# Kernel tuning notes

Measured on AMD Instinct MI355X. Metric: run time of the kernel, lower is better.

Reference implementation:

```python
import jax, jax.numpy as jnp
import numpy as np

DIM = 768
NUM_HEADS = 12
HEAD_DIM = DIM // NUM_HEADS
ALL_HEAD_DIM = HEAD_DIM * NUM_HEADS
SCALE = HEAD_DIM ** -0.5


def setup_inputs() -> dict:
    key = jax.random.key(0)
    k1, k2, k3, k4 = jax.random.split(key, 4)
    B, N = 8, 1024
    x = jax.random.normal(k1, (B, N, DIM), dtype=jnp.float32)
    # qkv_bias=False -> no qkv bias; proj has bias (nn.Linear default)
    w_qkv = jax.random.normal(k2, (DIM, 3 * ALL_HEAD_DIM), dtype=jnp.float32) * (DIM ** -0.5)
    w_proj = jax.random.normal(k3, (ALL_HEAD_DIM, DIM), dtype=jnp.float32) * (ALL_HEAD_DIM ** -0.5)
    b_proj = jax.random.normal(k4, (DIM,), dtype=jnp.float32) * 0.02
    return {"x": x, "w_qkv": w_qkv, "w_proj": w_proj, "b_proj": b_proj}


def reference(x, w_qkv, w_proj, b_proj):
    B, N, C = x.shape
    qkv = (x @ w_qkv).reshape(B, N, 3, NUM_HEADS, HEAD_DIM)
    qkv = jnp.transpose(qkv, (2, 0, 3, 1, 4))  # [3, B, H, N, D]
    q, k, v = qkv[0], qkv[1], qkv[2]
    attn = jax.nn.softmax(jnp.einsum('bhnd,bhmd->bhnm', q * SCALE, k), axis=-1)
    out = jnp.einsum('bhnm,bhmd->bhnd', attn, v)  # [B, H, N, D]
    out = jnp.transpose(out, (0, 2, 1, 3)).reshape(B, N, ALL_HEAD_DIM)
    return out @ w_proj + b_proj
```

## Files before the change

kernel.cpp:

```cpp
#include <hip/hip_runtime.h>
#include <hip/hip_bf16.h>

#define NH 12
#define HD 64
#define SEQ 1024
#define BATCH 8
#define DIM 768
#define QKVN 2304
#define ROWS 8192

typedef __bf16 bf16x8 __attribute__((ext_vector_type(8)));
typedef float f32x4 __attribute__((ext_vector_type(4)));
typedef unsigned short u16x8 __attribute__((ext_vector_type(8)));
typedef unsigned short u16x4 __attribute__((ext_vector_type(4)));
typedef short s16x4 __attribute__((ext_vector_type(4)));

__device__ __forceinline__ unsigned short f2bf(float f) {
  union { float f; unsigned int u; } c; c.f = f;
  unsigned int u = c.u;
  u += 0x7fffu + ((u >> 16) & 1u);
  return (unsigned short)(u >> 16);
}

__device__ __forceinline__ unsigned int pk_bf16(float a, float b) {
  union { __hip_bfloat162 h; unsigned int w; } u;
  u.h = __float22bfloat162_rn(float2{a, b});
  return u.w;
}

__device__ __forceinline__ float exp2_fast(float x) {
  float r;
  asm("v_exp_f32 %0, %1" : "=v"(r) : "v"(x));
  return r;
}

__device__ __forceinline__ void gload_lds16(const unsigned short* g, unsigned short* l) {
  __builtin_amdgcn_global_load_lds(
      (const __attribute__((address_space(1))) void*)g,
      (__attribute__((address_space(3))) void*)l, 16, 0, 0);
}

__device__ __forceinline__ void tr_tile(const float* __restrict__ src, unsigned short* __restrict__ dst,
                                        int R, int C, int bx, int by, float tile[32][33]) {
  int tx = threadIdx.x & 31, ty = threadIdx.x >> 5;
  int c0 = bx * 32, r0 = by * 32;
#pragma unroll
  for (int i = 0; i < 4; ++i)
    tile[ty + i * 8][tx] = src[(size_t)(r0 + ty + i * 8) * C + c0 + tx];
  __syncthreads();
#pragma unroll
  for (int i = 0; i < 4; ++i)
    dst[(size_t)(c0 + ty + i * 8) * R + r0 + tx] = f2bf(tile[tx][ty + i * 8]);
}

__global__ void prep_kernel(const float* __restrict__ x, unsigned short* __restrict__ xb,
                            const float* __restrict__ w_qkv, unsigned short* __restrict__ wqkvT,
                            const float* __restrict__ w_proj, unsigned short* __restrict__ wprojT) {
  __shared__ float tile[32][33];
  int blk = blockIdx.x;
  if (blk < 6144) {
    int i = blk * 256 + threadIdx.x;
    float4 v = ((const float4*)x)[i];
    unsigned int lo = pk_bf16(v.x, v.y), hi = pk_bf16(v.z, v.w);
    union { unsigned int w[2]; u16x4 o; } u; u.w[0] = lo; u.w[1] = hi;
    ((u16x4*)xb)[i] = u.o;
  } else if (blk < 6144 + 1728) {
    int t = blk - 6144;
    tr_tile(w_qkv, wqkvT, DIM, QKVN, t % 72, t / 72, tile);
  } else {
    int t = blk - 6144 - 1728;
    tr_tile(w_proj, wprojT, DIM, DIM, t % 24, t / 24, tile);
  }
}

template <bool BF16_OUT, bool SCALE_Q>
__global__ __launch_bounds__(256, 3) void gemm192(
    const unsigned short* __restrict__ A, const unsigned short* __restrict__ BT,
    void* __restrict__ Cout, const float* __restrict__ bias,
    int M, int N, int K, int nbyXCD) {
  __shared__ unsigned short As[2][128 * 32];
  __shared__ unsigned short Bs[2][192 * 32];
  const int tid = threadIdx.x;
  const int wave = tid >> 6, lane = tid & 63, quad = lane >> 4, l16 = lane & 15;
  const int wm = wave >> 1, wn = wave & 1;
  const int g = blockIdx.x & 7, bi = blockIdx.x >> 3;
  const int by = g * nbyXCD + (bi % nbyXCD);
  const int bx = bi / nbyXCD;
  const int bm = by * 128, bn = bx * 192;

  const int r0 = tid >> 2, kc0 = (tid & 3) * 8;
  const unsigned short* Ag = A + (size_t)(bm + r0) * K + kc0;
  const unsigned short* Bg = BT + (size_t)(bn + r0) * K + kc0;
  unsigned short* AsB = &As[0][0];
  unsigned short* BsB = &Bs[0][0];
  const int wdst = (tid & ~63) * 8;

#define STAGE_G(kt, b) do {                                                   \
    int koff_ = (kt) * 32;                                                    \
    gload_lds16(Ag + koff_,                    AsB + (b) * 4096 + wdst);      \
    gload_lds16(Ag + koff_ + (size_t)64 * K,   AsB + (b) * 4096 + wdst + 2048);\
    gload_lds16(Bg + koff_,                    BsB + (b) * 6144 + wdst);      \
    gload_lds16(Bg + koff_ + (size_t)64 * K,   BsB + (b) * 6144 + wdst + 2048);\
    gload_lds16(Bg + koff_ + (size_t)128 * K,  BsB + (b) * 6144 + wdst + 4096);\
  } while (0)

  f32x4 zero4 = {0.f, 0.f, 0.f, 0.f};
  f32x4 acc[4][6];
#pragma unroll
  for (int i = 0; i < 4; ++i)
#pragma unroll
    for (int j = 0; j < 6; ++j) acc[i][j] = zero4;

  const int nkt = K >> 5;
  STAGE_G(0, 0);
  for (int kt = 0; kt < nkt; ++kt) {
    __syncthreads();
    if (kt + 1 < nkt) STAGE_G(kt + 1, (kt + 1) & 1);
    const unsigned short* Ab = AsB + (kt & 1) * 4096;
    const unsigned short* Bb = BsB + (kt & 1) * 6144;
    bf16x8 af[4], bf[6];
#pragma unroll
    for (int mt = 0; mt < 4; ++mt)
      af[mt] = *(const bf16x8*)&Ab[(wm * 64 + mt * 16 + l16) * 32 + quad * 8];
#pragma unroll
    for (int nt = 0; nt < 6; ++nt)
      bf[nt] = *(const bf16x8*)&Bb[(wn * 96 + nt * 16 + l16) * 32 + quad * 8];
#pragma unroll
    for (int mt = 0; mt < 4; ++mt)
#pragma unroll
      for (int nt = 0; nt < 6; ++nt)
        acc[mt][nt] = __builtin_amdgcn_mfma_f32_16x16x32_bf16(af[mt], bf[nt], acc[mt][nt], 0, 0, 0);
  }
#undef STAGE_G

#pragma unroll
  for (int mt = 0; mt < 4; ++mt)
#pragma unroll
    for (int nt = 0; nt < 6; ++nt) {
      int col = bn + wn * 96 + nt * 16 + l16;
      float bv = BF16_OUT ? 0.f : bias[col];
      float scl = (SCALE_Q && col < DIM) ? 0.18033688011112042f : 1.0f;
#pragma unroll
      for (int r = 0; r < 4; ++r) {
        int row = bm + wm * 64 + mt * 16 + quad * 4 + r;
        float v = acc[mt][nt][r];
        if (BF16_OUT)
          ((unsigned short*)Cout)[(size_t)row * N + col] = f2bf(v * scl);
        else
          ((float*)Cout)[(size_t)row * N + col] = v + bv;
      }
    }
}

__global__ __launch_bounds__(256, 5) void gemm64_proj(
    const unsigned short* __restrict__ A, const unsigned short* __restrict__ BT,
    float* __restrict__ Cout, const float* __restrict__ bias,
    int M, int N, int K, int nbyXCD) {
  __shared__ unsigned short As[2][128 * 32];
  __shared__ unsigned short Bs[2][64 * 32];
  const int tid = threadIdx.x;
  const int wave = tid >> 6, lane = tid & 63, quad = lane >> 4, l16 = lane & 15;
  const int g = blockIdx.x & 7, bi = blockIdx.x >> 3;
  const int by = g * nbyXCD + (bi % nbyXCD);
  const int bx = bi / nbyXCD;
  const int bm = by * 128, bn = bx * 64;

  const int r0 = tid >> 2, kc0 = (tid & 3) * 8;
  const unsigned short* Ag = A + (size_t)(bm + r0) * K + kc0;
  const unsigned short* Bg = BT + (size_t)(bn + r0) * K + kc0;
  unsigned short* AsB = &As[0][0];
  unsigned short* BsB = &Bs[0][0];
  const int wdst = (tid & ~63) * 8;

#define STAGE_P(kt, b) do {                                                    \
    int koff_ = (kt) * 32;                                                     \
    gload_lds16(Ag + koff_,                  AsB + (b) * 4096 + wdst);         \
    gload_lds16(Ag + koff_ + (size_t)64 * K, AsB + (b) * 4096 + wdst + 2048);  \
    gload_lds16(Bg + koff_,                  BsB + (b) * 2048 + wdst);         \
  } while (0)

  f32x4 zero4 = {0.f, 0.f, 0.f, 0.f};
  f32x4 acc[2][4];
#pragma unroll
  for (int i = 0; i < 2; ++i)
#pragma unroll
    for (int j = 0; j < 4; ++j) acc[i][j] = zero4;

  const int nkt = K >> 5;
  STAGE_P(0, 0);
  for (int kt = 0; kt < nkt; ++kt) {
    __syncthreads();
    if (kt + 1 < nkt) STAGE_P(kt + 1, (kt + 1) & 1);
    const unsigned short* Ab = AsB + (kt & 1) * 4096;
    const unsigned short* Bb = BsB + (kt & 1) * 2048;
    bf16x8 af[2], bf[4];
#pragma unroll
    for (int mt = 0; mt < 2; ++mt)
      af[mt] = *(const bf16x8*)&Ab[(wave * 32 + mt * 16 + l16) * 32 + quad * 8];
#pragma unroll
    for (int nt = 0; nt < 4; ++nt)
      bf[nt] = *(const bf16x8*)&Bb[(nt * 16 + l16) * 32 + quad * 8];
#pragma unroll
    for (int mt = 0; mt < 2; ++mt)
#pragma unroll
      for (int nt = 0; nt < 4; ++nt)
        acc[mt][nt] = __builtin_amdgcn_mfma_f32_16x16x32_bf16(af[mt], bf[nt], acc[mt][nt], 0, 0, 0);
  }
#undef STAGE_P

#pragma unroll
  for (int mt = 0; mt < 2; ++mt)
#pragma unroll
    for (int nt = 0; nt < 4; ++nt) {
      int col = bn + nt * 16 + l16;
      float bv = bias[col];
#pragma unroll
      for (int r = 0; r < 4; ++r) {
        int row = bm + wave * 32 + mt * 16 + quad * 4 + r;
        Cout[(size_t)row * N + col] = acc[mt][nt][r] + bv;
      }
    }
}

#define VS 76
__global__ __launch_bounds__(512, 6) void attn_kernel(
    const unsigned short* __restrict__ qkv, unsigned short* __restrict__ out) {
  __shared__ unsigned short Ks[2][64 * 64];
  __shared__ unsigned short Vts[2][64 * VS];

  const int tid = threadIdx.x;
  const int wave = tid >> 6, lane = tid & 63, quad = lane >> 4, l16 = lane & 15;
  const int x = blockIdx.x;
  const int qt = (x >> 3) & 7;
  const int bh = (x & 7) + 8 * (x >> 6);
  const int b = bh / NH, h = bh % NH;
  const int qcol = h * HD, kcol = DIM + h * HD, vcol = 2 * DIM + h * HD;
  const int rowQ0 = b * SEQ + qt * 128;
  const int rowKV0 = b * SEQ;

  const int kk_s = tid >> 8, rem_s = tid & 255, n_s = rem_s >> 2, kc_s = rem_s & 3;
  const unsigned short* kgp = qkv + (size_t)(rowKV0 + n_s) * QKVN + kcol + kk_s * 32 + kc_s * 8;
  unsigned short* klp = &Ks[0][0] + (tid & ~63) * 8;
  const int vn = tid & 63, vd0 = (tid >> 6) * 8;
  const unsigned short* vgp = qkv + (size_t)(rowKV0 + vn) * QKVN + vcol + vd0;

  bf16x8 qf[2];
  {
    const unsigned short* qp = qkv + (size_t)(rowQ0 + wave * 16 + l16) * QKVN + qcol + quad * 8;
    qf[0] = *(const bf16x8*)qp;
    qf[1] = *(const bf16x8*)(qp + 32);
  }

  gload_lds16(kgp, klp);
  {
    u16x8 v0 = *(const u16x8*)vgp;
    unsigned short* vb = &Vts[0][0];
#pragma unroll
    for (int e = 0; e < 8; ++e)
      vb[(vd0 + e) * VS + vn] = v0[e];
  }

  f32x4 zero4 = {0.f, 0.f, 0.f, 0.f};
  f32x4 o[4];
#pragma unroll
  for (int dt = 0; dt < 4; ++dt) o[dt] = zero4;
  float lsum = 0.f;

  for (int jt = 0; jt < 16; ++jt) {
    __syncthreads();
    u16x8 vnext;
    if (jt < 15) {
      gload_lds16(kgp + (size_t)(jt + 1) * 64 * QKVN, klp + ((jt + 1) & 1) * 4096);
      vnext = *(const u16x8*)(vgp + (size_t)(jt + 1) * 64 * QKVN);
    }

    const unsigned short* Kb = &Ks[jt & 1][0];
    const unsigned short* Vb = &Vts[jt & 1][0];

    f32x4 s[4];
#pragma unroll
    for (int nt = 0; nt < 4; ++nt) s[nt] = zero4;
    __builtin_amdgcn_s_setprio(1);
#pragma unroll
    for (int kk = 0; kk < 2; ++kk)
#pragma unroll
      for (int nt = 0; nt < 4; ++nt) {
        bf16x8 kf = *(const bf16x8*)&Kb[kk * 2048 + (nt * 16 + l16) * 32 + quad * 8];
        s[nt] = __builtin_amdgcn_mfma_f32_16x16x32_bf16(kf, qf[kk], s[nt], 0, 0, 0);
      }
    __builtin_amdgcn_s_setprio(0);

    s16x4 pf[4];
#pragma unroll
    for (int nt = 0; nt < 4; ++nt) {
      float p0 = exp2_fast(s[nt][0]);
      float p1 = exp2_fast(s[nt][1]);
      float p2 = exp2_fast(s[nt][2]);
      float p3 = exp2_fast(s[nt][3]);
      lsum += (p0 + p1) + (p2 + p3);
      union { unsigned int w[2]; s16x4 v; } u;
      u.w[0] = pk_bf16(p0, p1);
      u.w[1] = pk_bf16(p2, p3);
      pf[nt] = u.v;
    }

    __builtin_amdgcn_s_setprio(1);
#pragma unroll
    for (int nt = 0; nt < 4; ++nt)
#pragma unroll
      for (int dt = 0; dt < 4; ++dt) {
        s16x4 vv = *(const s16x4*)&Vb[(dt * 16 + l16) * VS + nt * 16 + quad * 4];
        o[dt] = __builtin_amdgcn_mfma_f32_16x16x16bf16_1k(pf[nt], vv, o[dt], 0, 0, 0);
      }
    __builtin_amdgcn_s_setprio(0);

    if (jt < 15) {
      unsigned short* vb = &Vts[(jt + 1) & 1][0];
#pragma unroll
      for (int e = 0; e < 8; ++e)
        vb[(vd0 + e) * VS + vn] = vnext[e];
    }
  }

  float l = lsum;
  l += __shfl_xor(l, 16);
  l += __shfl_xor(l, 32);
#pragma unroll
  for (int r = 0; r < 4; ++r) {
    float inv = 1.f / __shfl(l, quad * 4 + r);
    int row = rowQ0 + wave * 16 + quad * 4 + r;
#pragma unroll
    for (int dt = 0; dt < 4; ++dt)
      out[(size_t)row * DIM + h * HD + dt * 16 + l16] = f2bf(o[dt][r] * inv);
  }
}

extern "C" void kernel_launch(void* const* d_in, const int* in_sizes, int n_in,
                              void* d_out, int out_size, void* d_ws, size_t ws_size,
                              hipStream_t stream) {
  const float* x = (const float*)d_in[0];
  const float* w_qkv = (const float*)d_in[1];
  const float* w_proj = (const float*)d_in[2];
  const float* b_proj = (const float*)d_in[3];
  float* outp = (float*)d_out;

  unsigned short* xb = (unsigned short*)d_ws;
  unsigned short* wqkvT = xb + (size_t)ROWS * DIM;
  unsigned short* wprojT = wqkvT + (size_t)QKVN * DIM;
  unsigned short* qkvb = wprojT + (size_t)DIM * DIM;
  unsigned short* attnb = xb;

  prep_kernel<<<dim3(6144 + 1728 + 576), 256, 0, stream>>>(x, xb, w_qkv, wqkvT, w_proj, wprojT);
  gemm192<true, true><<<dim3(768), 256, 0, stream>>>(xb, wqkvT, qkvb, nullptr, ROWS, QKVN, DIM, 8);
  attn_kernel<<<dim3(8 * 96), 512, 0, stream>>>(qkvb, attnb);
  gemm64_proj<<<dim3(768), 256, 0, stream>>>(attnb, wprojT, outp, b_proj, ROWS, DIM, DIM, 8);
}
```

Measured before the change: 178.5 us.

## Double K-tile depth in proj GEMM with swizzled LDS and widen attention KV tile

The projection GEMM now stages 64-wide K slices instead of 32, using an XOR-swizzled LDS layout to avoid bank conflicts. This halves the number of barriers and iterations per tile. The attention kernel now processes 128 keys per iteration instead of 64, halving the loop trip count and its syncs. In exchange both kernels use more LDS and registers, and their occupancy bounds are lowered to match.

Result: slower. 182.1 us (+2.0%).

```diff
diff --git a/kernel.cpp b/kernel.cpp
--- a/kernel.cpp
+++ b/kernel.cpp
@@ -152,12 +152,12 @@
     }
 }
 
-__global__ __launch_bounds__(256, 5) void gemm64_proj(
+__global__ __launch_bounds__(256, 4) void gemm64_proj(
     const unsigned short* __restrict__ A, const unsigned short* __restrict__ BT,
     float* __restrict__ Cout, const float* __restrict__ bias,
     int M, int N, int K, int nbyXCD) {
-  __shared__ unsigned short As[2][128 * 32];
-  __shared__ unsigned short Bs[2][64 * 32];
+  __shared__ unsigned short As[2][128 * 64];
+  __shared__ unsigned short Bs[2][64 * 64];
   const int tid = threadIdx.x;
   const int wave = tid >> 6, lane = tid & 63, quad = lane >> 4, l16 = lane & 15;
   const int g = blockIdx.x & 7, bi = blockIdx.x >> 3;
@@ -165,18 +165,22 @@
   const int bx = bi / nbyXCD;
   const int bm = by * 128, bn = bx * 64;
 
-  const int r0 = tid >> 2, kc0 = (tid & 3) * 8;
-  const unsigned short* Ag = A + (size_t)(bm + r0) * K + kc0;
-  const unsigned short* Bg = BT + (size_t)(bn + r0) * K + kc0;
+  const int r0 = tid >> 3;
+  const int csw = ((tid & 7) ^ (r0 & 7)) * 8;
+  const unsigned short* Ag = A + (size_t)(bm + r0) * K + csw;
+  const unsigned short* Bg = BT + (size_t)(bn + r0) * K + csw;
   unsigned short* AsB = &As[0][0];
   unsigned short* BsB = &Bs[0][0];
   const int wdst = (tid & ~63) * 8;
 
-#define STAGE_P(kt, b) do {                                                    \
-    int koff_ = (kt) * 32;                                                     \
-    gload_lds16(Ag + koff_,                  AsB + (b) * 4096 + wdst);         \
-    gload_lds16(Ag + koff_ + (size_t)64 * K, AsB + (b) * 4096 + wdst + 2048);  \
-    gload_lds16(Bg + koff_,                  BsB + (b) * 2048 + wdst);         \
+#define STAGE_P(kt, b) do {                                                     \
+    int koff_ = (kt) * 64;                                                      \
+    gload_lds16(Ag + koff_,                   AsB + (b) * 8192 + wdst);         \
+    gload_lds16(Ag + koff_ + (size_t)32 * K,  AsB + (b) * 8192 + wdst + 2048);  \
+    gload_lds16(Ag + koff_ + (size_t)64 * K,  AsB + (b) * 8192 + wdst + 4096);  \
+    gload_lds16(Ag + koff_ + (size_t)96 * K,  AsB + (b) * 8192 + wdst + 6144);  \
+    gload_lds16(Bg + koff_,                   BsB + (b) * 4096 + wdst);         \
+    gload_lds16(Bg + koff_ + (size_t)32 * K,  BsB + (b) * 4096 + wdst + 2048);  \
   } while (0)
 
   f32x4 zero4 = {0.f, 0.f, 0.f, 0.f};
@@ -186,25 +190,29 @@
 #pragma unroll
     for (int j = 0; j < 4; ++j) acc[i][j] = zero4;
 
-  const int nkt = K >> 5;
+  const int nkt = K >> 6;
   STAGE_P(0, 0);
   for (int kt = 0; kt < nkt; ++kt) {
     __syncthreads();
     if (kt + 1 < nkt) STAGE_P(kt + 1, (kt + 1) & 1);
-    const unsigned short* Ab = AsB + (kt & 1) * 4096;
-    const unsigned short* Bb = BsB + (kt & 1) * 2048;
-    bf16x8 af[2], bf[4];
-#pragma unroll
-    for (int mt = 0; mt < 2; ++mt)
-      af[mt] = *(const bf16x8*)&Ab[(wave * 32 + mt * 16 + l16) * 32 + quad * 8];
-#pragma unroll
-    for (int nt = 0; nt < 4; ++nt)
-      bf[nt] = *(const bf16x8*)&Bb[(nt * 16 + l16) * 32 + quad * 8];
-#pragma unroll
-    for (int mt = 0; mt < 2; ++mt)
+    const unsigned short* Ab = AsB + (kt & 1) * 8192;
+    const unsigned short* Bb = BsB + (kt & 1) * 4096;
+#pragma unroll
+    for (int kk = 0; kk < 2; ++kk) {
+      const int pc = ((kk * 4 + quad) ^ (l16 & 7)) * 8;
+      bf16x8 af[2], bf[4];
+#pragma unroll
+      for (int mt = 0; mt < 2; ++mt)
+        af[mt] = *(const bf16x8*)&Ab[(wave * 32 + mt * 16 + l16) * 64 + pc];
 #pragma unroll
       for (int nt = 0; nt < 4; ++nt)
-        acc[mt][nt] = __builtin_amdgcn_mfma_f32_16x16x32_bf16(af[mt], bf[nt], acc[mt][nt], 0, 0, 0);
+        bf[nt] = *(const bf16x8*)&Bb[(nt * 16 + l16) * 64 + pc];
+#pragma unroll
+      for (int mt = 0; mt < 2; ++mt)
+#pragma unroll
+        for (int nt = 0; nt < 4; ++nt)
+          acc[mt][nt] = __builtin_amdgcn_mfma_f32_16x16x32_bf16(af[mt], bf[nt], acc[mt][nt], 0, 0, 0);
+    }
   }
 #undef STAGE_P
 
@@ -222,11 +230,11 @@
     }
 }
 
-#define VS 76
-__global__ __launch_bounds__(512, 6) void attn_kernel(
+#define VS2 132
+__global__ __launch_bounds__(512, 4) void attn_kernel(
     const unsigned short* __restrict__ qkv, unsigned short* __restrict__ out) {
-  __shared__ unsigned short Ks[2][64 * 64];
-  __shared__ unsigned short Vts[2][64 * VS];
+  __shared__ unsigned short Ks[2][2 * 128 * 32];
+  __shared__ unsigned short Vts[2][64 * VS2];
 
   const int tid = threadIdx.x;
   const int wave = tid >> 6, lane = tid & 63, quad = lane >> 4, l16 = lane & 15;
@@ -238,10 +246,10 @@
   const int rowQ0 = b * SEQ + qt * 128;
   const int rowKV0 = b * SEQ;
 
-  const int kk_s = tid >> 8, rem_s = tid & 255, n_s = rem_s >> 2, kc_s = rem_s & 3;
-  const unsigned short* kgp = qkv + (size_t)(rowKV0 + n_s) * QKVN + kcol + kk_s * 32 + kc_s * 8;
+  const int n_s = tid >> 2, kc_s = tid & 3;
+  const unsigned short* kgp = qkv + (size_t)(rowKV0 + n_s) * QKVN + kcol + kc_s * 8;
   unsigned short* klp = &Ks[0][0] + (tid & ~63) * 8;
-  const int vn = tid & 63, vd0 = (tid >> 6) * 8;
+  const int vn = tid & 127, vd0 = (tid >> 7) * 16;
   const unsigned short* vgp = qkv + (size_t)(rowKV0 + vn) * QKVN + vcol + vd0;
 
   bf16x8 qf[2];
@@ -252,12 +260,16 @@
   }
 
   gload_lds16(kgp, klp);
+  gload_lds16(kgp + 32, klp + 4096);
   {
-    u16x8 v0 = *(const u16x8*)vgp;
+    u16x8 v0a = *(const u16x8*)vgp;
+    u16x8 v0b = *(const u16x8*)(vgp + 8);
     unsigned short* vb = &Vts[0][0];
 #pragma unroll
-    for (int e = 0; e < 8; ++e)
-      vb[(vd0 + e) * VS + vn] = v0[e];
+    for (int e = 0; e < 8; ++e) {
+      vb[(vd0 + e) * VS2 + vn] = v0a[e];
+      vb[(vd0 + 8 + e) * VS2 + vn] = v0b[e];
+    }
   }
 
   f32x4 zero4 = {0.f, 0.f, 0.f, 0.f};
@@ -266,33 +278,37 @@
   for (int dt = 0; dt < 4; ++dt) o[dt] = zero4;
   float lsum = 0.f;
 
-  for (int jt = 0; jt < 16; ++jt) {
+  for (int jt = 0; jt < 8; ++jt) {
     __syncthreads();
-    u16x8 vnext;
-    if (jt < 15) {
-      gload_lds16(kgp + (size_t)(jt + 1) * 64 * QKVN, klp + ((jt + 1) & 1) * 4096);
-      vnext = *(const u16x8*)(vgp + (size_t)(jt + 1) * 64 * QKVN);
+    u16x8 vna, vnb;
+    if (jt < 7) {
+      const size_t goff = (size_t)(jt + 1) * 128 * QKVN;
+      unsigned short* kd = klp + ((jt + 1) & 1) * 8192;
+      gload_lds16(kgp + goff, kd);
+      gload_lds16(kgp + goff + 32, kd + 4096);
+      vna = *(const u16x8*)(vgp + goff);
+      vnb = *(const u16x8*)(vgp + goff + 8);
     }
 
     const unsigned short* Kb = &Ks[jt & 1][0];
     const unsigned short* Vb = &Vts[jt & 1][0];
 
-    f32x4 s[4];
-#pragma unroll
-    for (int nt = 0; nt < 4; ++nt) s[nt] = zero4;
+    f32x4 s[8];
+#pragma unroll
+    for (int nt = 0; nt < 8; ++nt) s[nt] = zero4;
     __builtin_amdgcn_s_setprio(1);
 #pragma unroll
     for (int kk = 0; kk < 2; ++kk)
 #pragma unroll
-      for (int nt = 0; nt < 4; ++nt) {
-        bf16x8 kf = *(const bf16x8*)&Kb[kk * 2048 + (nt * 16 + l16) * 32 + quad * 8];
+      for (int nt = 0; nt < 8; ++nt) {
+        bf16x8 kf = *(const bf16x8*)&Kb[kk * 4096 + (nt * 16 + l16) * 32 + quad * 8];
         s[nt] = __builtin_amdgcn_mfma_f32_16x16x32_bf16(kf, qf[kk], s[nt], 0, 0, 0);
       }
     __builtin_amdgcn_s_setprio(0);
 
-    s16x4 pf[4];
-#pragma unroll
-    for (int nt = 0; nt < 4; ++nt) {
+    s16x4 pf[8];
+#pragma unroll
+    for (int nt = 0; nt < 8; ++nt) {
       float p0 = exp2_fast(s[nt][0]);
       float p1 = exp2_fast(s[nt][1]);
       float p2 = exp2_fast(s[nt][2]);
@@ -306,19 +322,21 @@
 
     __builtin_amdgcn_s_setprio(1);
 #pragma unroll
-    for (int nt = 0; nt < 4; ++nt)
+    for (int nt = 0; nt < 8; ++nt)
 #pragma unroll
       for (int dt = 0; dt < 4; ++dt) {
-        s16x4 vv = *(const s16x4*)&Vb[(dt * 16 + l16) * VS + nt * 16 + quad * 4];
+        s16x4 vv = *(const s16x4*)&Vb[(dt * 16 + l16) * VS2 + nt * 16 + quad * 4];
         o[dt] = __builtin_amdgcn_mfma_f32_16x16x16bf16_1k(pf[nt], vv, o[dt], 0, 0, 0);
       }
     __builtin_amdgcn_s_setprio(0);
 
-    if (jt < 15) {
+    if (jt < 7) {
       unsigned short* vb = &Vts[(jt + 1) & 1][0];
 #pragma unroll
-      for (int e = 0; e < 8; ++e)
-        vb[(vd0 + e) * VS + vn] = vnext[e];
+      for (int e = 0; e < 8; ++e) {
+        vb[(vd0 + e) * VS2 + vn] = vna[e];
+        vb[(vd0 + 8 + e) * VS2 + vn] = vnb[e];
+      }
     }
   }
 
```

## Triple-buffer LDS staging in QKV and proj GEMMs with explicit vmcnt waits

Applied to the files above, without the earlier changes.

Both bf16 GEMM kernels go from double-buffered to triple-buffered LDS, with tiles prefetched two k-steps ahead. The full __syncthreads (which waits for all outstanding loads) is replaced by a partial s_waitcnt vmcnt plus s_barrier, so the next tile's global-to-LDS loads stay in flight across the barrier. This is meant to hide global memory latency better. In exchange it uses 1.5x the LDS, so the proj kernel's launch bound drops from 5 to 3 blocks per CU and occupancy may fall.

Result: slower. 187.7 us (+5.2%).

```diff
diff --git a/kernel.cpp b/kernel.cpp
--- a/kernel.cpp
+++ b/kernel.cpp
@@ -78,8 +78,8 @@
     const unsigned short* __restrict__ A, const unsigned short* __restrict__ BT,
     void* __restrict__ Cout, const float* __restrict__ bias,
     int M, int N, int K, int nbyXCD) {
-  __shared__ unsigned short As[2][128 * 32];
-  __shared__ unsigned short Bs[2][192 * 32];
+  __shared__ unsigned short As[3][128 * 32];
+  __shared__ unsigned short Bs[3][192 * 32];
   const int tid = threadIdx.x;
   const int wave = tid >> 6, lane = tid & 63, quad = lane >> 4, l16 = lane & 15;
   const int wm = wave >> 1, wn = wave & 1;
@@ -113,11 +113,16 @@
 
   const int nkt = K >> 5;
   STAGE_G(0, 0);
+  STAGE_G(1, 1);
+  int cur = 0, stg = 2;
   for (int kt = 0; kt < nkt; ++kt) {
-    __syncthreads();
-    if (kt + 1 < nkt) STAGE_G(kt + 1, (kt + 1) & 1);
-    const unsigned short* Ab = AsB + (kt & 1) * 4096;
-    const unsigned short* Bb = BsB + (kt & 1) * 6144;
+    if (kt + 1 < nkt) asm volatile("s_waitcnt vmcnt(5)" ::: "memory");
+    else              asm volatile("s_waitcnt vmcnt(0)" ::: "memory");
+    __builtin_amdgcn_s_barrier();
+    __builtin_amdgcn_sched_barrier(0);
+    if (kt + 2 < nkt) STAGE_G(kt + 2, stg);
+    const unsigned short* Ab = AsB + cur * 4096;
+    const unsigned short* Bb = BsB + cur * 6144;
     bf16x8 af[4], bf[6];
 #pragma unroll
     for (int mt = 0; mt < 4; ++mt)
@@ -130,6 +135,8 @@
 #pragma unroll
       for (int nt = 0; nt < 6; ++nt)
         acc[mt][nt] = __builtin_amdgcn_mfma_f32_16x16x32_bf16(af[mt], bf[nt], acc[mt][nt], 0, 0, 0);
+    cur = (cur == 2) ? 0 : cur + 1;
+    stg = (stg == 2) ? 0 : stg + 1;
   }
 #undef STAGE_G
 
@@ -152,12 +159,12 @@
     }
 }
 
-__global__ __launch_bounds__(256, 5) void gemm64_proj(
+__global__ __launch_bounds__(256, 3) void gemm64_proj(
     const unsigned short* __restrict__ A, const unsigned short* __restrict__ BT,
     float* __restrict__ Cout, const float* __restrict__ bias,
     int M, int N, int K, int nbyXCD) {
-  __shared__ unsigned short As[2][128 * 32];
-  __shared__ unsigned short Bs[2][64 * 32];
+  __shared__ unsigned short As[3][128 * 32];
+  __shared__ unsigned short Bs[3][64 * 32];
   const int tid = threadIdx.x;
   const int wave = tid >> 6, lane = tid & 63, quad = lane >> 4, l16 = lane & 15;
   const int g = blockIdx.x & 7, bi = blockIdx.x >> 3;
@@ -188,11 +195,16 @@
 
   const int nkt = K >> 5;
   STAGE_P(0, 0);
+  STAGE_P(1, 1);
+  int cur = 0, stg = 2;
   for (int kt = 0; kt < nkt; ++kt) {
-    __syncthreads();
-    if (kt + 1 < nkt) STAGE_P(kt + 1, (kt + 1) & 1);
-    const unsigned short* Ab = AsB + (kt & 1) * 4096;
-    const unsigned short* Bb = BsB + (kt & 1) * 2048;
+    if (kt + 1 < nkt) asm volatile("s_waitcnt vmcnt(3)" ::: "memory");
+    else              asm volatile("s_waitcnt vmcnt(0)" ::: "memory");
+    __builtin_amdgcn_s_barrier();
+    __builtin_amdgcn_sched_barrier(0);
+    if (kt + 2 < nkt) STAGE_P(kt + 2, stg);
+    const unsigned short* Ab = AsB + cur * 4096;
+    const unsigned short* Bb = BsB + cur * 2048;
     bf16x8 af[2], bf[4];
 #pragma unroll
     for (int mt = 0; mt < 2; ++mt)
@@ -205,6 +217,8 @@
 #pragma unroll
       for (int nt = 0; nt < 4; ++nt)
         acc[mt][nt] = __builtin_amdgcn_mfma_f32_16x16x32_bf16(af[mt], bf[nt], acc[mt][nt], 0, 0, 0);
+    cur = (cur == 2) ? 0 : cur + 1;
+    stg = (stg == 2) ? 0 : stg + 1;
   }
 #undef STAGE_P
 
```
